# Performance work log

Hardware: AMD Instinct MI355X
Metric: run time of the kernel (lower is better)

## Reference

```python
import jax, jax.numpy as jnp
import numpy as np

NUM_BLOCKS = 18
ANCHOR_IDX = (1, 4, 9)
TARGET_IDX = (11, 14, 17)
DIM = 512
HID = max(32, DIM // 4)  # 128
A = len(ANCHOR_IDX)


def setup_inputs() -> dict:
    key = jax.random.key(0)
    ks = jax.random.split(key, 8)
    B, H, W, C = 32, 14, 14, DIM
    scale = 1.0 / np.sqrt(C)
    x = jax.random.normal(ks[0], (B, H, W, C), dtype=jnp.float32)
    # 18 per-block linear transforms standing in for orig_stage.blocks
    block_w = jax.random.normal(ks[1], (NUM_BLOCKS, C, C), dtype=jnp.float32) * scale
    block_b = jax.random.normal(ks[2], (NUM_BLOCKS, C), dtype=jnp.float32) * 0.01
    # per-target-index ChannelGating routers (3 of them)
    fc1_w = jax.random.normal(ks[3], (len(TARGET_IDX), C, HID), dtype=jnp.float32) * scale
    fc1_b = jnp.zeros((len(TARGET_IDX), HID), dtype=jnp.float32)
    # original zero-inits fc2; use small random values so all paths are exercised
    fc2_w = jax.random.normal(ks[4], (len(TARGET_IDX), HID, A * C), dtype=jnp.float32) * 0.02
    fc2_b = jax.random.normal(ks[5], (len(TARGET_IDX), A * C), dtype=jnp.float32) * 0.02
    gammas = jnp.full((len(TARGET_IDX),), 0.1, dtype=jnp.float32)
    return {"x": x, "block_w": block_w, "block_b": block_b,
            "fc1_w": fc1_w, "fc1_b": fc1_b, "fc2_w": fc2_w, "fc2_b": fc2_b,
            "gammas": gammas}


def reference(x, block_w, block_b, fc1_w, fc1_b, fc2_w, fc2_b, gammas):
    C = x.shape[-1]
    anchors = []
    for i in range(NUM_BLOCKS):
        # block: dense linear + GELU  [B,H,W,C] @ [C,C]
        nx = jax.nn.gelu(jnp.einsum('bhwc,cd->bhwd', x, block_w[i]) + block_b[i])
        if i in TARGET_IDX:
            t = TARGET_IDX.index(i)
            # ChannelGating: global mean pool -> 2-layer MLP -> softmax over anchors
            pooled = nx.mean(axis=(1, 2))                       # [B,C]
            h = jax.nn.gelu(pooled @ fc1_w[t] + fc1_b[t])       # [B,HID]
            logits = (h @ fc2_w[t] + fc2_b[t]).reshape(-1, A, C)  # [B,A,C]
            gates = jax.nn.softmax(logits, axis=1)              # softmax over anchors
            # weighted anchor feature sum, gates broadcast over H,W
            anc = jnp.stack(anchors, axis=1)                    # [B,A,H,W,C]
            routed = jnp.einsum('bac,bahwc->bhwc', gates, anc)
            nx = nx + gammas[t] * routed
        x = nx
        if i in ANCHOR_IDX:
            anchors.append(x)
    return x
```

## Files before the change

### kernel.cpp

```cpp
#include <hip/hip_runtime.h>

#define B_   32
#define HW_  196
#define C_   512
#define M_   (B_*HW_)
#define HID_ 128
#define NBLK 18

typedef _Float16 f16;
typedef _Float16 f16x2 __attribute__((ext_vector_type(2)));
typedef _Float16 f16x4 __attribute__((ext_vector_type(4)));
typedef _Float16 f16x8 __attribute__((ext_vector_type(8)));
typedef float    f32x4 __attribute__((ext_vector_type(4)));

__device__ __forceinline__ float gelu_f(float x) {
    float t = tanhf(0.7978845608028654f * (x + 0.044715f * x * x * x));
    return 0.5f * x * (1.0f + t);
}

__device__ __forceinline__ void gl16(const void* g, void* l) {
    __builtin_amdgcn_global_load_lds((const __attribute__((address_space(1))) unsigned*)g,
                                     (__attribute__((address_space(3))) unsigned*)l, 16, 0, 0);
}

__global__ __launch_bounds__(256) void conv_w(const float* __restrict__ W,
                                              f16* __restrict__ Wt) {
    __shared__ f16 sh[64][72];
    const int blk = blockIdx.z, k0 = blockIdx.x * 64, n0 = blockIdx.y * 64;
    const int tid = threadIdx.x;
    const float* Wb = W + (size_t)blk * C_ * C_;
    #pragma unroll
    for (int i = 0; i < 4; ++i) {
        int s = tid + i * 256, r = s >> 4, c4 = (s & 15) << 2;
        float4 v = *(const float4*)&Wb[(size_t)(k0 + r) * C_ + n0 + c4];
        sh[r][c4 + 0] = (f16)v.x; sh[r][c4 + 1] = (f16)v.y;
        sh[r][c4 + 2] = (f16)v.z; sh[r][c4 + 3] = (f16)v.w;
    }
    __syncthreads();
    #pragma unroll
    for (int i = 0; i < 2; ++i) {
        int s = tid + i * 256, r = s >> 3, c8 = (s & 7) << 3;
        f16x8 o;
        #pragma unroll
        for (int j = 0; j < 8; ++j) o[j] = sh[c8 + j][r];
        *(f16x8*)&Wt[(size_t)blk * C_ * C_ + (size_t)(n0 + r) * C_ + k0 + c8] = o;
    }
}

__global__ __launch_bounds__(256) void conv_x(const float* __restrict__ in,
                                              f16* __restrict__ out) {
    int i = blockIdx.x * 256 + threadIdx.x;
    float4 a = ((const float4*)in)[i];
    f16x4 o; o[0] = (f16)a.x; o[1] = (f16)a.y; o[2] = (f16)a.z; o[3] = (f16)a.w;
    ((f16x4*)out)[i] = o;
}

__global__ __launch_bounds__(256) void zero_pooled(float* __restrict__ p) {
    p[blockIdx.x * 256 + threadIdx.x] = 0.f;
}

#define BM 64
#define BN 64
#define BK 64
#define NKT (C_ / BK)
__global__ __launch_bounds__(256, 4) void gemm_f16(
    const f16* __restrict__ A, const f16* __restrict__ Wt,
    const float* __restrict__ ball, int blk, f16* __restrict__ out,
    float* __restrict__ pooled)
{
    __shared__ f16 As[2][BM * BK];
    __shared__ f16 Ws[2][BN * BK];
    __shared__ float spool[2][BN];
    const int tid = threadIdx.x;
    const int wave = tid >> 6, lane = tid & 63;
    const int m15 = lane & 15, q = lane >> 4;
    const int wr = wave >> 1, wc = wave & 1;

    const int lin  = blockIdx.x + 98 * blockIdx.y;
    const int tile = (lin & 7) * 98 + (lin >> 3);
    const int rb   = tile >> 3, cb = tile & 7;
    const int row0 = rb * BM, col0 = cb * BN;

    const f16* Wb = Wt + (size_t)blk * C_ * C_;
    const float* bias = ball + (size_t)blk * C_;

    const int srow = lane >> 3;
    const int scol = ((lane & 7) ^ (srow & 7)) << 3;
    const f16* aSrc[2]; const f16* wSrc[2];
    f16* aDst[2][2]; f16* wDst[2][2];
    #pragma unroll
    for (int i = 0; i < 2; ++i) {
        int ch = wave * 2 + i;
        aSrc[i] = A  + (size_t)(row0 + ch * 8 + srow) * C_ + scol;
        wSrc[i] = Wb + (size_t)(col0 + ch * 8 + srow) * C_ + scol;
        aDst[0][i] = &As[0][ch * 512]; aDst[1][i] = &As[1][ch * 512];
        wDst[0][i] = &Ws[0][ch * 512]; wDst[1][i] = &Ws[1][ch * 512];
    }

    f32x4 acc[2][2];
    #pragma unroll
    for (int i = 0; i < 2; ++i)
        #pragma unroll
        for (int j = 0; j < 2; ++j) acc[i][j] = (f32x4)0.f;

    #pragma unroll
    for (int i = 0; i < 2; ++i) { gl16(aSrc[i], aDst[0][i]); gl16(wSrc[i], wDst[0][i]); }

    #pragma unroll
    for (int kt = 0; kt < NKT; ++kt) {
        __syncthreads();
        int cur = kt & 1;
        if (kt + 1 < NKT) {
            int nxt = cur ^ 1, koff = (kt + 1) * BK;
            #pragma unroll
            for (int i = 0; i < 2; ++i) {
                gl16(aSrc[i] + koff, aDst[nxt][i]);
                gl16(wSrc[i] + koff, wDst[nxt][i]);
            }
        }
        const f16* Ab = &As[cur][0];
        const f16* Bb = &Ws[cur][0];
        #pragma unroll
        for (int kk = 0; kk < BK; kk += 32) {
            f16x8 af[2], bf[2];
            #pragma unroll
            for (int i = 0; i < 2; ++i) {
                int r = wr * 32 + i * 16 + m15;
                int c = (kk >> 3) + q;
                af[i] = *(const f16x8*)&Ab[r * 64 + ((c ^ (r & 7)) << 3)];
            }
            #pragma unroll
            for (int j = 0; j < 2; ++j) {
                int r = wc * 32 + j * 16 + m15;
                int c = (kk >> 3) + q;
                bf[j] = *(const f16x8*)&Bb[r * 64 + ((c ^ (r & 7)) << 3)];
            }
            __builtin_amdgcn_s_setprio(1);
            #pragma unroll
            for (int i = 0; i < 2; ++i)
                #pragma unroll
                for (int j = 0; j < 2; ++j)
                    acc[i][j] = __builtin_amdgcn_mfma_f32_16x16x32_f16(af[i], bf[j], acc[i][j], 0, 0, 0);
            __builtin_amdgcn_s_setprio(0);
        }
    }

    const bool doPool = (pooled != nullptr);
    if (doPool) {
        if (tid < 2 * BN) ((float*)spool)[tid] = 0.f;
        __syncthreads();
    }
    const int bA = row0 / HW_;
    float ps[2][2] = {{0.f, 0.f}, {0.f, 0.f}};
    float bcol[2];
    #pragma unroll
    for (int j = 0; j < 2; ++j) bcol[j] = bias[col0 + wc * 32 + j * 16 + m15];
    #pragma unroll
    for (int i = 0; i < 2; ++i) {
        #pragma unroll
        for (int r = 0; r < 4; ++r) {
            int rloc = wr * 32 + i * 16 + q * 4 + r;
            int row = row0 + rloc;
            int slot = (row / HW_) - bA;
            #pragma unroll
            for (int j = 0; j < 2; ++j) {
                int col = col0 + wc * 32 + j * 16 + m15;
                float v = gelu_f(acc[i][j][r] + bcol[j]);
                out[(size_t)row * C_ + col] = (f16)v;
                if (doPool) ps[slot & 1][j] += v;
            }
        }
    }
    if (doPool) {
        #pragma unroll
        for (int s = 0; s < 2; ++s)
            #pragma unroll
            for (int j = 0; j < 2; ++j)
                atomicAdd(&spool[s][wc * 32 + j * 16 + m15], ps[s][j]);
        __syncthreads();
        if (tid < 2 * BN) {
            int slot = tid >> 6, colt = tid & 63;
            int b = bA + slot;
            int lastb = (row0 + BM - 1) / HW_;
            if (b <= lastb)
                atomicAdd(&pooled[(size_t)b * C_ + col0 + colt], spool[slot][colt]);
        }
    }
}

__global__ __launch_bounds__(256) void gate_kernel(float* __restrict__ pooled,
    const float* __restrict__ fc1w, const float* __restrict__ fc1b,
    const float* __restrict__ fc2w, const float* __restrict__ fc2b,
    int t, float* __restrict__ gates)
{
    __shared__ float sp[C_];
    __shared__ float sh2[2][HID_];
    __shared__ float sh[HID_];
    const int b = blockIdx.x, tid = threadIdx.x;

    float2 pv = *(const float2*)&pooled[b * C_ + 2 * tid];
    sp[2 * tid]     = pv.x * (1.f / 196.f);
    sp[2 * tid + 1] = pv.y * (1.f / 196.f);
    *(float2*)&pooled[b * C_ + 2 * tid] = make_float2(0.f, 0.f);
    __syncthreads();

    {
        int half = tid >> 7, hh = tid & 127;
        const float* w = fc1w + (size_t)t * C_ * HID_ + hh;
        float s = 0.f;
        int c0 = half * 256;
        for (int c = c0; c < c0 + 256; ++c) s += sp[c] * w[(size_t)c * HID_];
        sh2[half][hh] = s;
    }
    __syncthreads();
    if (tid < HID_) sh[tid] = gelu_f(sh2[0][tid] + sh2[1][tid] + fc1b[t * HID_ + tid]);
    __syncthreads();

    #pragma unroll
    for (int cc = 0; cc < 2; ++cc) {
        int c = tid + cc * 256;
        const float* w2 = fc2w + (size_t)t * HID_ * (3 * C_) + c;
        float l0 = fc2b[t * 3 * C_ + c];
        float l1 = fc2b[t * 3 * C_ + C_ + c];
        float l2 = fc2b[t * 3 * C_ + 2 * C_ + c];
        for (int j = 0; j < HID_; ++j) {
            float h = sh[j];
            const float* r = w2 + (size_t)j * 3 * C_;
            l0 += h * r[0];
            l1 += h * r[C_];
            l2 += h * r[2 * C_];
        }
        float m  = fmaxf(l0, fmaxf(l1, l2));
        float e0 = expf(l0 - m), e1 = expf(l1 - m), e2 = expf(l2 - m);
        float inv = 1.f / (e0 + e1 + e2);
        gates[(size_t)b * 3 * C_ + c]          = e0 * inv;
        gates[(size_t)b * 3 * C_ + C_ + c]     = e1 * inv;
        gates[(size_t)b * 3 * C_ + 2 * C_ + c] = e2 * inv;
    }
}

__global__ __launch_bounds__(256) void routed_add_kernel(f16* __restrict__ nx,
    const f16* __restrict__ a0, const f16* __restrict__ a1, const f16* __restrict__ a2,
    const float* __restrict__ gates, const float* __restrict__ gammas, int t,
    float* __restrict__ outf)
{
    int v = blockIdx.x * 256 + threadIdx.x;
    int idx = v * 8;
    int c = idx & (C_ - 1);
    int b = idx / (HW_ * C_);
    const float* g = gates + (size_t)b * 3 * C_ + c;
    float gamma = gammas[t];
    f16x8 xn = ((const f16x8*)nx)[v];
    f16x8 x0 = ((const f16x8*)a0)[v];
    f16x8 x1 = ((const f16x8*)a1)[v];
    f16x8 x2 = ((const f16x8*)a2)[v];
    float r[8];
    #pragma unroll
    for (int e = 0; e < 8; ++e)
        r[e] = (float)xn[e] + gamma * (g[e] * (float)x0[e] + g[C_ + e] * (float)x1[e]
                                       + g[2 * C_ + e] * (float)x2[e]);
    if (outf) {
        float4* o = (float4*)&outf[idx];
        o[0] = make_float4(r[0], r[1], r[2], r[3]);
        o[1] = make_float4(r[4], r[5], r[6], r[7]);
    } else {
        f16x8 o;
        #pragma unroll
        for (int e = 0; e < 8; ++e) o[e] = (f16)r[e];
        ((f16x8*)nx)[v] = o;
    }
}

extern "C" void kernel_launch(void* const* d_in, const int* in_sizes, int n_in,
                              void* d_out, int out_size, void* d_ws, size_t ws_size,
                              hipStream_t stream)
{
    const float* x      = (const float*)d_in[0];
    const float* blockw = (const float*)d_in[1];
    const float* blockb = (const float*)d_in[2];
    const float* fc1w   = (const float*)d_in[3];
    const float* fc1b   = (const float*)d_in[4];
    const float* fc2w   = (const float*)d_in[5];
    const float* fc2b   = (const float*)d_in[6];
    const float* gammas = (const float*)d_in[7];
    float* out = (float*)d_out;

    const size_t NB = (size_t)M_ * C_;
    f16* Wt = (f16*)d_ws;
    f16* P0 = Wt + (size_t)NBLK * C_ * C_;
    f16* P1 = P0 + NB;
    f16* A0 = P0 + 2 * NB;
    f16* A1 = P0 + 3 * NB;
    f16* A2 = P0 + 4 * NB;
    float* pooled = (float*)(P0 + 5 * NB);
    float* gates  = pooled + B_ * C_;

    zero_pooled<<<B_ * C_ / 256, 256, 0, stream>>>(pooled);
    conv_w<<<dim3(8, 8, NBLK), 256, 0, stream>>>(blockw, Wt);
    conv_x<<<(int)(NB / 1024), 256, 0, stream>>>(x, P1);

    const f16* ins[NBLK]  = {P1, P0, A0, P0, P1, A1, P0, P1, P0, P1, A2, P0, P1, P0, P1, P0, P1, P0};
    f16*       outs[NBLK] = {P0, A0, P0, P1, A1, P0, P1, P0, P1, A2, P0, P1, P0, P1, P0, P1, P0, P1};

    for (int i = 0; i < NBLK; ++i) {
        int t = (i == 11) ? 0 : (i == 14) ? 1 : (i == 17) ? 2 : -1;
        gemm_f16<<<dim3(M_ / BM, C_ / BN), 256, 0, stream>>>(
            ins[i], Wt, blockb, i, outs[i], (t >= 0) ? pooled : (float*)nullptr);
        if (t >= 0) {
            gate_kernel<<<B_, 256, 0, stream>>>(pooled, fc1w, fc1b, fc2w, fc2b, t, gates);
            routed_add_kernel<<<(int)(NB / 2048), 256, 0, stream>>>(
                outs[i], A0, A1, A2, gates, gammas, t,
                (t == 2) ? out : (float*)nullptr);
        }
    }
}
```

Measured before the change: 385.3 us.

## Fuse routed anchor add into next GEMM's A-tile staging and merge pooled zeroing

The gated residual add after blocks 11 and 14 moves out of a separate elementwise kernel and into the A-operand staging of the following GEMM. That GEMM loads the raw activation, the three anchors and the gates, combines them in registers and writes the result to LDS. Zeroing of the pooled buffer is folded into the input conversion kernel, and only the final routed add stays as a standalone kernel. This removes launches and a full read-modify-write pass over the activation. In exchange, the gated GEMMs give up async global-to-LDS loads for A and redo the routing math once per column tile, multiplying anchor and gate reads.

```diff
diff --git a/kernel.cpp b/kernel.cpp
--- a/kernel.cpp
+++ b/kernel.cpp
@@ -48,15 +48,13 @@
 }
 
 __global__ __launch_bounds__(256) void conv_x(const float* __restrict__ in,
-                                              f16* __restrict__ out) {
+                                              f16* __restrict__ out,
+                                              float* __restrict__ pooled) {
     int i = blockIdx.x * 256 + threadIdx.x;
+    if (blockIdx.x < 64) pooled[i] = 0.f;
     float4 a = ((const float4*)in)[i];
     f16x4 o; o[0] = (f16)a.x; o[1] = (f16)a.y; o[2] = (f16)a.z; o[3] = (f16)a.w;
     ((f16x4*)out)[i] = o;
-}
-
-__global__ __launch_bounds__(256) void zero_pooled(float* __restrict__ p) {
-    p[blockIdx.x * 256 + threadIdx.x] = 0.f;
 }
 
 #define BM 64
@@ -66,7 +64,9 @@
 __global__ __launch_bounds__(256, 4) void gemm_f16(
     const f16* __restrict__ A, const f16* __restrict__ Wt,
     const float* __restrict__ ball, int blk, f16* __restrict__ out,
-    float* __restrict__ pooled)
+    float* __restrict__ pooled,
+    const f16* __restrict__ ra0, const f16* __restrict__ ra1, const f16* __restrict__ ra2,
+    const float* __restrict__ gates, const float* __restrict__ gammas, int tprev)
 {
     __shared__ f16 As[2][BM * BK];
     __shared__ f16 Ws[2][BN * BK];
@@ -83,19 +83,34 @@
 
     const f16* Wb = Wt + (size_t)blk * C_ * C_;
     const float* bias = ball + (size_t)blk * C_;
+    const bool gated = (tprev >= 0);
 
     const int srow = lane >> 3;
     const int scol = ((lane & 7) ^ (srow & 7)) << 3;
     const f16* aSrc[2]; const f16* wSrc[2];
     f16* aDst[2][2]; f16* wDst[2][2];
+    int ldsoff[2];
+    const f16 *g0p[2], *g1p[2], *g2p[2];
+    const float* gbp[2];
+    float gamma = 0.f;
     #pragma unroll
     for (int i = 0; i < 2; ++i) {
         int ch = wave * 2 + i;
-        aSrc[i] = A  + (size_t)(row0 + ch * 8 + srow) * C_ + scol;
+        int rg = row0 + ch * 8 + srow;
+        aSrc[i] = A  + (size_t)rg * C_ + scol;
         wSrc[i] = Wb + (size_t)(col0 + ch * 8 + srow) * C_ + scol;
         aDst[0][i] = &As[0][ch * 512]; aDst[1][i] = &As[1][ch * 512];
         wDst[0][i] = &Ws[0][ch * 512]; wDst[1][i] = &Ws[1][ch * 512];
-    }
+        ldsoff[i] = (ch * 8 + srow) * 64 + ((lane & 7) << 3);
+        if (gated) {
+            int b = rg / HW_;
+            g0p[i] = ra0 + (size_t)rg * C_ + scol;
+            g1p[i] = ra1 + (size_t)rg * C_ + scol;
+            g2p[i] = ra2 + (size_t)rg * C_ + scol;
+            gbp[i] = gates + (size_t)b * 3 * C_ + scol;
+        }
+    }
+    if (gated) gamma = gammas[tprev];
 
     f32x4 acc[2][2];
     #pragma unroll
@@ -103,8 +118,42 @@
         #pragma unroll
         for (int j = 0; j < 2; ++j) acc[i][j] = (f32x4)0.f;
 
-    #pragma unroll
-    for (int i = 0; i < 2; ++i) { gl16(aSrc[i], aDst[0][i]); gl16(wSrc[i], wDst[0][i]); }
+    auto stageA = [&](int bb, int koff) {
+        if (!gated) {
+            #pragma unroll
+            for (int i = 0; i < 2; ++i) gl16(aSrc[i] + koff, aDst[bb][i]);
+        } else {
+            #pragma unroll
+            for (int i = 0; i < 2; ++i) {
+                f16x8 raw = *(const f16x8*)(aSrc[i] + koff);
+                f16x8 v0  = *(const f16x8*)(g0p[i] + koff);
+                f16x8 v1  = *(const f16x8*)(g1p[i] + koff);
+                f16x8 v2  = *(const f16x8*)(g2p[i] + koff);
+                float4 G0a = *(const float4*)(gbp[i] + koff);
+                float4 G0b = *(const float4*)(gbp[i] + koff + 4);
+                float4 G1a = *(const float4*)(gbp[i] + C_ + koff);
+                float4 G1b = *(const float4*)(gbp[i] + C_ + koff + 4);
+                float4 G2a = *(const float4*)(gbp[i] + 2 * C_ + koff);
+                float4 G2b = *(const float4*)(gbp[i] + 2 * C_ + koff + 4);
+                const float* g0 = &G0a.x; const float* g1 = &G1a.x; const float* g2 = &G2a.x;
+                f16x8 res;
+                #pragma unroll
+                for (int e = 0; e < 4; ++e)
+                    res[e] = (f16)((float)raw[e] + gamma * ((&G0a.x)[e] * (float)v0[e]
+                              + (&G1a.x)[e] * (float)v1[e] + (&G2a.x)[e] * (float)v2[e]));
+                #pragma unroll
+                for (int e = 0; e < 4; ++e)
+                    res[4 + e] = (f16)((float)raw[4 + e] + gamma * ((&G0b.x)[e] * (float)v0[4 + e]
+                              + (&G1b.x)[e] * (float)v1[4 + e] + (&G2b.x)[e] * (float)v2[4 + e]));
+                *(f16x8*)&As[bb][ldsoff[i]] = res;
+                (void)g0; (void)g1; (void)g2;
+            }
+        }
+    };
+
+    stageA(0, 0);
+    #pragma unroll
+    for (int i = 0; i < 2; ++i) gl16(wSrc[i], wDst[0][i]);
 
     #pragma unroll
     for (int kt = 0; kt < NKT; ++kt) {
@@ -112,11 +161,9 @@
         int cur = kt & 1;
         if (kt + 1 < NKT) {
             int nxt = cur ^ 1, koff = (kt + 1) * BK;
-            #pragma unroll
-            for (int i = 0; i < 2; ++i) {
-                gl16(aSrc[i] + koff, aDst[nxt][i]);
-                gl16(wSrc[i] + koff, wDst[nxt][i]);
-            }
+            stageA(nxt, koff);
+            #pragma unroll
+            for (int i = 0; i < 2; ++i) gl16(wSrc[i] + koff, wDst[nxt][i]);
         }
         const f16* Ab = &As[cur][0];
         const f16* Bb = &Ws[cur][0];
@@ -239,9 +286,9 @@
     }
 }
 
-__global__ __launch_bounds__(256) void routed_add_kernel(f16* __restrict__ nx,
+__global__ __launch_bounds__(256) void routed_final_kernel(const f16* __restrict__ nx,
     const f16* __restrict__ a0, const f16* __restrict__ a1, const f16* __restrict__ a2,
-    const float* __restrict__ gates, const float* __restrict__ gammas, int t,
+    const float* __restrict__ gates, const float* __restrict__ gammas,
     float* __restrict__ outf)
 {
     int v = blockIdx.x * 256 + threadIdx.x;
@@ -249,7 +296,7 @@
     int c = idx & (C_ - 1);
     int b = idx / (HW_ * C_);
     const float* g = gates + (size_t)b * 3 * C_ + c;
-    float gamma = gammas[t];
+    float gamma = gammas[2];
     f16x8 xn = ((const f16x8*)nx)[v];
     f16x8 x0 = ((const f16x8*)a0)[v];
     f16x8 x1 = ((const f16x8*)a1)[v];
@@ -259,16 +306,9 @@
     for (int e = 0; e < 8; ++e)
         r[e] = (float)xn[e] + gamma * (g[e] * (float)x0[e] + g[C_ + e] * (float)x1[e]
                                        + g[2 * C_ + e] * (float)x2[e]);
-    if (outf) {
-        float4* o = (float4*)&outf[idx];
-        o[0] = make_float4(r[0], r[1], r[2], r[3]);
-        o[1] = make_float4(r[4], r[5], r[6], r[7]);
-    } else {
-        f16x8 o;
-        #pragma unroll
-        for (int e = 0; e < 8; ++e) o[e] = (f16)r[e];
-        ((f16x8*)nx)[v] = o;
-    }
+    float4* o = (float4*)&outf[idx];
+    o[0] = make_float4(r[0], r[1], r[2], r[3]);
+    o[1] = make_float4(r[4], r[5], r[6], r[7]);
 }
 
 extern "C" void kernel_launch(void* const* d_in, const int* in_sizes, int n_in,
@@ -295,22 +335,21 @@
     float* pooled = (float*)(P0 + 5 * NB);
     float* gates  = pooled + B_ * C_;
 
-    zero_pooled<<<B_ * C_ / 256, 256, 0, stream>>>(pooled);
     conv_w<<<dim3(8, 8, NBLK), 256, 0, stream>>>(blockw, Wt);
-    conv_x<<<(int)(NB / 1024), 256, 0, stream>>>(x, P1);
+    conv_x<<<(int)(NB / 1024), 256, 0, stream>>>(x, P1, pooled);
 
     const f16* ins[NBLK]  = {P1, P0, A0, P0, P1, A1, P0, P1, P0, P1, A2, P0, P1, P0, P1, P0, P1, P0};
     f16*       outs[NBLK] = {P0, A0, P0, P1, A1, P0, P1, P0, P1, A2, P0, P1, P0, P1, P0, P1, P0, P1};
 
     for (int i = 0; i < NBLK; ++i) {
         int t = (i == 11) ? 0 : (i == 14) ? 1 : (i == 17) ? 2 : -1;
+        int tprev = (i == 12) ? 0 : (i == 15) ? 1 : -1;
         gemm_f16<<<dim3(M_ / BM, C_ / BN), 256, 0, stream>>>(
-            ins[i], Wt, blockb, i, outs[i], (t >= 0) ? pooled : (float*)nullptr);
-        if (t >= 0) {
+            ins[i], Wt, blockb, i, outs[i], (t >= 0) ? pooled : (float*)nullptr,
+            A0, A1, A2, gates, gammas, tprev);
+        if (t >= 0)
             gate_kernel<<<B_, 256, 0, stream>>>(pooled, fc1w, fc1b, fc2w, fc2b, t, gates);
-            routed_add_kernel<<<(int)(NB / 2048), 256, 0, stream>>>(
-                outs[i], A0, A1, A2, gates, gammas, t,
-                (t == 2) ? out : (float*)nullptr);
-        }
-    }
-}
+    }
+    routed_final_kernel<<<(int)(NB / 2048), 256, 0, stream>>>(
+        outs[17], A0, A1, A2, gates, gammas, out);
+}
```

Result: slower. 405.5 us (+5.2%).
